# Performance work log

Measured on AMD Instinct MI355X. Metric: run time of the kernel, lower is better.

The kernel has to match this reference:

```python
import jax, jax.numpy as jnp
import numpy as np

NEG_SLOPE = 0.2  # LeakyReLU slope
PAD = 1          # padding for all 3x3 convs (kernel_size // 2)
K = 9            # 3x3 deformable kernel taps


def _conv2d(x, w, b):
    # x: (B,Cin,H,W), w: (Cout,Cin,3,3) -> (B,Cout,H,W), stride 1, SAME pad
    y = jax.lax.conv_general_dilated(x, w, (1, 1), 'SAME',
                                     dimension_numbers=('NCHW', 'OIHW', 'NCHW'))
    return y + b[None, :, None, None]


def _leaky(x):
    return jnp.where(x >= 0, x, NEG_SLOPE * x)


def _deform_conv(x, offset, w, b):
    # torchvision DeformConv2d, kernel 3x3, stride 1, pad 1, no modulation.
    # x: (B,C,H,W); offset: (B, 2*K, H, W) ordered (dy,dx) per tap; w: (O,C,3,3)
    B, C, H, W = x.shape
    O = w.shape[0]
    off = offset.reshape(B, K, 2, H, W)
    ks = jnp.arange(K)
    ky = (ks // 3).astype(x.dtype)
    kx = (ks % 3).astype(x.dtype)
    iy = jnp.arange(H, dtype=x.dtype)
    ix = jnp.arange(W, dtype=x.dtype)
    # sampling locations: out_pos + tap_pos - pad + learned offset  -> (B,K,H,W)
    py = iy[None, None, :, None] + ky[None, :, None, None] - PAD + off[:, :, 0]
    px = ix[None, None, None, :] + kx[None, :, None, None] - PAD + off[:, :, 1]

    y0 = jnp.floor(py)
    x0 = jnp.floor(px)
    wy = py - y0
    wx = px - x0
    y0i = y0.astype(jnp.int32)
    x0i = x0.astype(jnp.int32)

    def gather(img, yi, xi):  # img: (C,H,W); yi,xi: (K,H,W) -> (C,K,H,W)
        return img[:, yi, xi]
    vgather = jax.vmap(gather)  # over batch

    def corner(yi, xi, wgt):
        valid = (yi >= 0) & (yi < H) & (xi >= 0) & (xi < W)
        yc = jnp.clip(yi, 0, H - 1)
        xc = jnp.clip(xi, 0, W - 1)
        v = vgather(x, yc, xc)  # (B,C,K,H,W)
        return v * (wgt * valid.astype(x.dtype))[:, None]

    val = (corner(y0i, x0i, (1 - wy) * (1 - wx))
           + corner(y0i, x0i + 1, (1 - wy) * wx)
           + corner(y0i + 1, x0i, wy * (1 - wx))
           + corner(y0i + 1, x0i + 1, wy * wx))  # (B,C,K,H,W)
    out = jnp.einsum('bckhw,ock->bohw', val, w.reshape(O, C, K))
    return out + b[None, :, None, None]


def _stage(x, cw, cb, ow, ob, dw, db):
    h = _leaky(_conv2d(x, cw, cb))      # plain conv + LeakyReLU
    off = _conv2d(h, ow, ob)            # offset prediction (18 channels)
    return _leaky(_deform_conv(h, off, dw, db))


def setup_inputs() -> dict:
    key = jax.random.key(0)
    keys = iter(jax.random.split(key, 32))

    def nrm(shape, scale):
        return jax.random.normal(next(keys), shape, jnp.float32) * scale

    inp = {'x': jax.random.normal(next(keys), (4, 64, 128, 128), jnp.float32)}
    specs = [(64, 128), (128, 128), (128, 64)]
    for i, (ci, co) in enumerate(specs, 1):
        inp[f's{i}_cw'] = nrm((co, ci, 3, 3), (ci * 9) ** -0.5)
        inp[f's{i}_cb'] = jnp.zeros((co,), jnp.float32)
        inp[f's{i}_ow'] = nrm((18, co, 3, 3), 0.1 * (co * 9) ** -0.5)  # small offsets
        inp[f's{i}_ob'] = jnp.zeros((18,), jnp.float32)
        inp[f's{i}_dw'] = nrm((co, co, 3, 3), (co * 9) ** -0.5)
        inp[f's{i}_db'] = jnp.zeros((co,), jnp.float32)
    return inp


def reference(x,
              s1_cw, s1_cb, s1_ow, s1_ob, s1_dw, s1_db,
              s2_cw, s2_cb, s2_ow, s2_ob, s2_dw, s2_db,
              s3_cw, s3_cb, s3_ow, s3_ob, s3_dw, s3_db):
    x = _stage(x, s1_cw, s1_cb, s1_ow, s1_ob, s1_dw, s1_db)
    x = _stage(x, s2_cw, s2_cb, s2_ow, s2_ob, s2_dw, s2_db)
    x = _stage(x, s3_cw, s3_cb, s3_ow, s3_ob, s3_dw, s3_db)
    return x
```

## Files before the change

kernel.cpp:

```cpp
#include <hip/hip_runtime.h>
#include <hip/hip_bf16.h>

#define HW 128
#define HW2 16384
#define NEG 0.2f

typedef __attribute__((ext_vector_type(8))) short short8;
typedef __attribute__((ext_vector_type(4))) float f32x4;
typedef __attribute__((ext_vector_type(2))) float f32x2;

__device__ __forceinline__ float lrelu(float v) { return v >= 0.f ? v : NEG * v; }
__device__ __forceinline__ unsigned short f2bf(float f) {
    unsigned int u = __float_as_uint(f);
    u = (u + 0x7fffu + ((u >> 16) & 1u)) >> 16;
    return (unsigned short)u;
}
__device__ __forceinline__ unsigned int pk2(float a, float b) {
    __hip_bfloat162 h = __float22bfloat162_rn(float2{a, b});
    return *(unsigned int*)&h;
}
__device__ __forceinline__ float2 upk(unsigned int u) {
    return float2{__uint_as_float(u << 16), __uint_as_float(u & 0xffff0000u)};
}
__device__ __forceinline__ f32x2 upkv(unsigned int u) {
    f32x2 r;
    r.x = __uint_as_float(u << 16);
    r.y = __uint_as_float(u & 0xffff0000u);
    return r;
}

struct WSeg { const float* s; unsigned short* d; int K9; int NMT; int validM; int n; };
struct WArgs { WSeg seg[9]; };

__global__ void wrepack_kernel(WArgs a)
{
    const WSeg sg = a.seg[blockIdx.y];
    int i = blockIdx.x * 256 + threadIdx.x;
    if (i >= sg.n) return;
    int cl = i & 7, lane = (i >> 3) & 63;
    int rest = i >> 9;
    int mt = rest % sg.NMT, gs = rest / sg.NMT;
    int st = gs % 3, g = gs / 3;
    int quad = lane >> 4, l15 = lane & 15;
    int co = mt * 16 + l15, tap = st * 4 + quad;
    unsigned short v = 0;
    if (tap < 9 && co < sg.validM)
        v = f2bf(sg.s[(size_t)co * sg.K9 + (g * 8 + cl) * 9 + tap]);
    sg.d[i] = v;
}

template <int MTW, int SRCF>
__global__ __launch_bounds__(256, 4) void fused_conv(
    const void* __restrict__ actv, const unsigned short* __restrict__ wpad,
    const float* __restrict__ bias, unsigned short* __restrict__ outb,
    float* __restrict__ outf, int Cin, int Cout, int mode)
{
    constexpr int PB = 136 * 16;
    constexpr int SMB = 64 * 136 * 2;
    __shared__ char smem[SMB];
    unsigned short* Es = (unsigned short*)smem;

    const int t = threadIdx.x;
    const int tile = blockIdx.x, b = blockIdx.z;
    const int lane = t & 63, wv = t >> 6, quad = lane >> 4, l15 = lane & 15;
    const int y0 = (tile >> 2) * 2, x0 = (tile & 3) * 32;
    const int ngrp = Cin >> 3;
    const int NSTR = (Cout >> 4) * 512;

    const bool sok = lane < 34;
    const int gy = y0 - 1 + wv, gx = x0 - 1 + lane;
    const bool pok = sok && gy >= 0 && gy < HW && gx >= 0 && gx < HW;
    const int gp = pok ? gy * HW + gx : 0;
    const int slot = wv * 34 + lane;

    const float* actf = (const float*)actv;
    const unsigned short* acth = (const unsigned short*)actv;
    const size_t bofs = (size_t)b * Cin * HW2;

    int baddr[3][4];
#pragma unroll
    for (int st = 0; st < 3; ++st) {
        int tap = st * 4 + quad; tap = tap > 8 ? 8 : tap;
        int ky = (tap * 11) >> 5, kx = tap - 3 * ky;
#pragma unroll
        for (int nt = 0; nt < 4; ++nt) {
            int p = nt * 16 + l15, ly = p >> 5, lx = p & 31;
            baddr[st][nt] = ((ly + ky) * 34 + lx + kx) * 16;
        }
    }
    size_t abase[MTW];
#pragma unroll
    for (int m = 0; m < MTW; ++m)
        abase[m] = (size_t)((wv * MTW + m) * 512 + lane * 8);

    f32x4 acc[MTW][4];
#pragma unroll
    for (int m = 0; m < MTW; ++m)
#pragma unroll
        for (int nt = 0; nt < 4; ++nt) acc[m][nt] = (f32x4)(0.f);

    auto load_grp = [&](int g) -> uint4 {
        uint4 u; u.x = u.y = u.z = u.w = 0;
        if (!pok) return u;
        if (SRCF == 1) {
            u = *(const uint4*)(acth + bofs + ((size_t)g * HW2 + gp) * 8);
        } else {
            const float* pl = actf + bofs + (size_t)(g * 8) * HW2 + gp;
            float v0 = pl[0], v1 = pl[HW2], v2 = pl[2 * HW2], v3 = pl[3 * HW2];
            float v4 = pl[4 * HW2], v5 = pl[5 * HW2], v6 = pl[6 * HW2], v7 = pl[7 * HW2];
            u.x = pk2(v0, v1); u.y = pk2(v2, v3);
            u.z = pk2(v4, v5); u.w = pk2(v6, v7);
        }
        return u;
    };

    short8 apre[MTW][3];
    auto loadA = [&](int g) {
#pragma unroll
        for (int st = 0; st < 3; ++st)
#pragma unroll
            for (int m = 0; m < MTW; ++m)
                apre[m][st] = *(const short8*)(wpad + (size_t)(g * 3 + st) * NSTR + abase[m]);
    };

    uint4 cur = load_grp(0);
    if (sok) *(uint4*)(smem + slot * 16) = cur;
    loadA(0);
    if (ngrp > 1) cur = load_grp(1);
    __syncthreads();

    for (int g = 0; g < ngrp; ++g) {
        char* pb = smem + (g & 1) * PB;
#pragma unroll
        for (int st = 0; st < 3; ++st) {
            short8 bfr[4];
#pragma unroll
            for (int nt = 0; nt < 4; ++nt)
                bfr[nt] = *(const short8*)(pb + baddr[st][nt]);
#pragma unroll
            for (int m = 0; m < MTW; ++m) {
                short8 a = apre[m][st];
#pragma unroll
                for (int nt = 0; nt < 4; ++nt)
                    acc[m][nt] = __builtin_amdgcn_mfma_f32_16x16x32_bf16(
                        a, bfr[nt], acc[m][nt], 0, 0, 0);
            }
        }
        if (g + 1 < ngrp) {
            if (sok) *(uint4*)(smem + ((g + 1) & 1) * PB + slot * 16) = cur;
            loadA(g + 1);
            if (g + 2 < ngrp) cur = load_grp(g + 2);
        }
        __syncthreads();
    }

    if (mode == 0) {
        constexpr int ESTR = 136;
#pragma unroll
        for (int m = 0; m < MTW; ++m) {
            int cb = (wv * MTW + m) * 16;
#pragma unroll
            for (int nt = 0; nt < 4; ++nt) {
                int px = nt * 16 + l15;
                int co = cb + quad * 4;
                unsigned int u0 = pk2(lrelu(acc[m][nt][0] + bias[co]),
                                      lrelu(acc[m][nt][1] + bias[co + 1]));
                unsigned int u1 = pk2(lrelu(acc[m][nt][2] + bias[co + 2]),
                                      lrelu(acc[m][nt][3] + bias[co + 3]));
                uint2 u; u.x = u0; u.y = u1;
                *(uint2*)&Es[px * ESTR + co] = u;
            }
        }
        __syncthreads();
        const int ng8 = Cout >> 3;
        unsigned short* ob = outb + (size_t)b * Cout * HW2;
        for (int tt = t; tt < 64 * ng8; tt += 256) {
            int cg = tt >> 6, px = tt & 63;
            int gp2 = (y0 + (px >> 5)) * HW + x0 + (px & 31);
            *(uint4*)(ob + ((size_t)cg * HW2 + gp2) * 8) =
                *(const uint4*)&Es[px * ESTR + cg * 8];
        }
    } else {
        float* of = outf + (size_t)b * 18 * HW2;
#pragma unroll
        for (int m = 0; m < MTW; ++m) {
            int cb = (wv * MTW + m) * 16;
#pragma unroll
            for (int nt = 0; nt < 4; ++nt) {
                int px = nt * 16 + l15;
                int gp2 = (y0 + (px >> 5)) * HW + x0 + (px & 31);
#pragma unroll
                for (int r = 0; r < 4; ++r) {
                    int co = cb + quad * 4 + r;
                    if (co < 18)
                        of[(size_t)co * HW2 + gp2] = acc[m][nt][r] + bias[co];
                }
            }
        }
    }
}

template <int MTW>
__global__ __launch_bounds__(256, 4) void fused_deform(
    const unsigned short* __restrict__ acth,
    const unsigned short* __restrict__ woff, const float* __restrict__ obias,
    const unsigned short* __restrict__ wpad, const float* __restrict__ bias,
    unsigned short* __restrict__ outb, float* __restrict__ outf,
    int Cin, int Cout, int mode)
{
    constexpr int PATW = 43, PATR = 8, PATP = PATR * PATW;
    constexpr int CSTR = 104;
    constexpr int PB = PATP * 16;
    constexpr int CB = 64 * CSTR * 2;
    constexpr int SMB = 2 * PB + 2 * CB;
    constexpr int OPB = 136 * 16;
    __shared__ char smem[SMB];
    unsigned short* Es = (unsigned short*)smem;

    const int t = threadIdx.x;
    const int tile = blockIdx.x, b = blockIdx.z;
    const int lane = t & 63, wv = t >> 6, quad = lane >> 4, l15 = lane & 15;
    const int y0 = (tile >> 2) * 2, x0 = (tile & 3) * 32;
    const int ngrp = Cin >> 3;
    const int NSTR = (Cout >> 4) * 512;
    const int py0 = y0 - 3, px0 = x0 - 5;
    const size_t bofs = (size_t)b * Cin * HW2;

    for (int i = t; i < 384; i += 256) {
        int bu = i / 192;
        int ii = i - 192 * bu;
        int p = ii / 3, j = ii - 3 * p;
        uint4 z; z.x = z.y = z.z = z.w = 0;
        *(uint4*)(smem + 2 * PB + bu * CB + (p * CSTR + 72 + j * 8) * 2) = z;
    }

    {
        float* offbuf = (float*)(smem + 2 * OPB);
        const bool asok = lane < 34;
        const int agy = y0 - 1 + wv, agx = x0 - 1 + lane;
        const bool apok = asok && agy >= 0 && agy < HW && agx >= 0 && agx < HW;
        const int agp = apok ? agy * HW + agx : 0;
        const int aslot = wv * 34 + lane;

        const int mtile = wv & 1, npair = wv >> 1;
        int obad[3][2];
#pragma unroll
        for (int st = 0; st < 3; ++st) {
            int tap = st * 4 + quad; tap = tap > 8 ? 8 : tap;
            int ky = (tap * 11) >> 5, kx = tap - 3 * ky;
#pragma unroll
            for (int nn = 0; nn < 2; ++nn) {
                int p = (2 * npair + nn) * 16 + l15, ly = p >> 5, lx = p & 31;
                obad[st][nn] = ((ly + ky) * 34 + lx + kx) * 16;
            }
        }
        const size_t oa0 = (size_t)(mtile * 512 + lane * 8);

        f32x4 oacc[2];
        oacc[0] = (f32x4)(0.f); oacc[1] = (f32x4)(0.f);
        short8 oapre[3];
        auto loadAO = [&](int g) {
#pragma unroll
            for (int st = 0; st < 3; ++st)
                oapre[st] = *(const short8*)(woff + (size_t)(g * 3 + st) * 1024 + oa0);
        };
        auto load_g = [&](int g) -> uint4 {
            uint4 u; u.x = u.y = u.z = u.w = 0;
            if (apok) u = *(const uint4*)(acth + bofs + ((size_t)g * HW2 + agp) * 8);
            return u;
        };

        uint4 cur = load_g(0);
        if (asok) *(uint4*)(smem + aslot * 16) = cur;
        loadAO(0);
        if (ngrp > 1) cur = load_g(1);
        __syncthreads();

        for (int g = 0; g < ngrp; ++g) {
            const char* pb = smem + (g & 1) * OPB;
#pragma unroll
            for (int st = 0; st < 3; ++st) {
                short8 a = oapre[st];
#pragma unroll
                for (int nn = 0; nn < 2; ++nn) {
                    short8 bf = *(const short8*)(pb + obad[st][nn]);
                    oacc[nn] = __builtin_amdgcn_mfma_f32_16x16x32_bf16(
                        a, bf, oacc[nn], 0, 0, 0);
                }
            }
            if (g + 1 < ngrp) {
                if (asok) *(uint4*)(smem + ((g + 1) & 1) * OPB + aslot * 16) = cur;
                loadAO(g + 1);
                if (g + 2 < ngrp) cur = load_g(g + 2);
            }
            __syncthreads();
        }

        {
            int co0 = mtile * 16 + quad * 4;
            if (co0 < 18) {
#pragma unroll
                for (int nn = 0; nn < 2; ++nn) {
                    int px = (2 * npair + nn) * 16 + l15;
#pragma unroll
                    for (int r = 0; r < 4; ++r)
                        if (co0 + r < 18)
                            offbuf[px * 20 + co0 + r] = oacc[nn][r] + obias[co0 + r];
                }
            }
        }
        __syncthreads();
    }
    const float* offbuf = (const float*)(smem + 2 * OPB);

    float w00[3], w01[3], w10[3], w11[3];
    int pbase[3], csad[3], svalid[3];
    int allin = 1;
    {
#pragma unroll
        for (int s = 0; s < 3; ++s) {
            int task = t + s * 256;
            svalid[s] = task < 576;
            int task2 = svalid[s] ? task : 0;
            int p = task2 / 9, k = task2 - 9 * p;
            int yy = y0 + (p >> 5), xx = x0 + (p & 31);
            float2 dd = *(const float2*)(offbuf + p * 20 + 2 * k);
            float dy = dd.x, dx = dd.y;
            float py = (float)(yy + k / 3 - 1) + dy;
            float px = (float)(xx + k % 3 - 1) + dx;
            float fy = floorf(py), fx = floorf(px);
            float wy = py - fy, wx = px - fx;
            int iy = (int)fy, ix = (int)fx;
            w00[s] = (1.f - wy) * (1.f - wx);
            w01[s] = (1.f - wy) * wx;
            w10[s] = wy * (1.f - wx);
            w11[s] = wy * wx;
            pbase[s] = ((iy - py0) * PATW + (ix - px0)) * 16;
            csad[s] = (p * CSTR + k * 8) * 2;
            bool ip = iy >= py0 && iy + 1 <= py0 + (PATR - 1)
                   && ix >= px0 && ix + 1 <= px0 + (PATW - 1);
            if (!ip) allin = 0;
        }
    }
    const int fast = __syncthreads_and(allin);

    const int s0 = wv * 86 + lane;
    const int r0 = s0 / PATW, c0_ = s0 - PATW * r0;
    const int gy0_ = py0 + r0, gx0_ = px0 + c0_;
    const bool ok0 = gy0_ >= 0 && gy0_ < HW && gx0_ >= 0 && gx0_ < HW;
    const int go0 = ok0 ? gy0_ * HW + gx0_ : 0;
    const bool has1 = lane < 22;
    const int s1 = wv * 86 + 64 + lane;
    const int r1 = s1 / PATW, c1_ = s1 - PATW * r1;
    const int gy1_ = py0 + r1, gx1_ = px0 + c1_;
    const bool ok1 = has1 && gy1_ >= 0 && gy1_ < HW && gx1_ >= 0 && gx1_ < HW;
    const int go1 = ok1 ? gy1_ * HW + gx1_ : 0;

    size_t abase[MTW];
#pragma unroll
    for (int m = 0; m < MTW; ++m)
        abase[m] = (size_t)((wv * MTW + m) * 512 + lane * 8);
    const int bb0 = l15 * (CSTR * 2) + quad * 16;

    f32x4 acc[MTW][4];
#pragma unroll
    for (int m = 0; m < MTW; ++m)
#pragma unroll
        for (int nt = 0; nt < 4; ++nt) acc[m][nt] = (f32x4)(0.f);

    short8 apre[MTW][3];
    auto loadA = [&](int g) {
#pragma unroll
        for (int st = 0; st < 3; ++st)
#pragma unroll
            for (int m = 0; m < MTW; ++m)
                apre[m][st] = *(const short8*)(wpad + (size_t)(g * 3 + st) * NSTR + abase[m]);
    };

    auto mfma_pre = [&](const char* cs) {
#pragma unroll
        for (int st = 0; st < 3; ++st) {
            short8 bfr[4];
#pragma unroll
            for (int nt = 0; nt < 4; ++nt)
                bfr[nt] = *(const short8*)(cs + bb0 + nt * 16 * (CSTR * 2) + st * 64);
#pragma unroll
            for (int m = 0; m < MTW; ++m) {
                short8 a = apre[m][st];
#pragma unroll
                for (int nt = 0; nt < 4; ++nt)
                    acc[m][nt] = __builtin_amdgcn_mfma_f32_16x16x32_bf16(
                        a, bfr[nt], acc[m][nt], 0, 0, 0);
            }
        }
    };

    if (fast) {
        uint4 u0, u1;
        u0.x = u0.y = u0.z = u0.w = 0; u1 = u0;
        if (ok0) u0 = *(const uint4*)(acth + bofs + (size_t)go0 * 8);
        if (ok1) u1 = *(const uint4*)(acth + bofs + (size_t)go1 * 8);
        *(uint4*)(smem + s0 * 16) = u0;
        if (has1) *(uint4*)(smem + s1 * 16) = u1;
        if (ngrp > 1) {
            u0.x = u0.y = u0.z = u0.w = 0; u1 = u0;
            if (ok0) u0 = *(const uint4*)(acth + bofs + ((size_t)HW2 + go0) * 8);
            if (ok1) u1 = *(const uint4*)(acth + bofs + ((size_t)HW2 + go1) * 8);
        }
        __syncthreads();

        for (int g = 0; g < ngrp; ++g) {
            const char* pb = smem + (g & 1) * PB;
            char* csW = smem + 2 * PB + (g & 1) * CB;

            if (g > 0)
                mfma_pre(smem + 2 * PB + ((g - 1) & 1) * CB);

#pragma unroll
            for (int s = 0; s < 3; ++s) {
                if (!svalid[s]) continue;
                const char* base = pb + pbase[s];
                uint4 c00 = *(const uint4*)base;
                uint4 c01 = *(const uint4*)(base + 16);
                uint4 c10 = *(const uint4*)(base + PATW * 16);
                uint4 c11 = *(const uint4*)(base + PATW * 16 + 16);
                f32x2 vw0 = (f32x2)(w00[s]), vw1 = (f32x2)(w01[s]);
                f32x2 vw2 = (f32x2)(w10[s]), vw3 = (f32x2)(w11[s]);
                f32x2 a0 = vw0 * upkv(c00.x) + vw1 * upkv(c01.x)
                         + vw2 * upkv(c10.x) + vw3 * upkv(c11.x);
                f32x2 a1 = vw0 * upkv(c00.y) + vw1 * upkv(c01.y)
                         + vw2 * upkv(c10.y) + vw3 * upkv(c11.y);
                f32x2 a2 = vw0 * upkv(c00.z) + vw1 * upkv(c01.z)
                         + vw2 * upkv(c10.z) + vw3 * upkv(c11.z);
                f32x2 a3 = vw0 * upkv(c00.w) + vw1 * upkv(c01.w)
                         + vw2 * upkv(c10.w) + vw3 * upkv(c11.w);
                uint4 ou;
                ou.x = pk2(a0.x, a0.y); ou.y = pk2(a1.x, a1.y);
                ou.z = pk2(a2.x, a2.y); ou.w = pk2(a3.x, a3.y);
                *(uint4*)(csW + csad[s]) = ou;
            }

            if (g + 1 < ngrp) {
                char* pn = smem + ((g + 1) & 1) * PB;
                *(uint4*)(pn + s0 * 16) = u0;
                if (has1) *(uint4*)(pn + s1 * 16) = u1;
            }
            loadA(g);
            if (g + 2 < ngrp) {
                u0.x = u0.y = u0.z = u0.w = 0; u1 = u0;
                if (ok0) u0 = *(const uint4*)(acth + bofs +
                                              ((size_t)(g + 2) * HW2 + go0) * 8);
                if (ok1) u1 = *(const uint4*)(acth + bofs +
                                              ((size_t)(g + 2) * HW2 + go1) * 8);
            }
            __syncthreads();
        }
        mfma_pre(smem + 2 * PB + ((ngrp - 1) & 1) * CB);
    } else {
        char* csW = smem + 2 * PB;
        for (int g = 0; g < ngrp; ++g) {
            const unsigned short* gb = acth + bofs + (size_t)g * HW2 * 8;
#pragma unroll
            for (int s = 0; s < 3; ++s) {
                if (!svalid[s]) continue;
                int task = t + s * 256;
                int p = task / 9, k = task - 9 * p;
                int yy = y0 + (p >> 5), xx = x0 + (p & 31);
                float2 dd = *(const float2*)(offbuf + p * 20 + 2 * k);
                float dy = dd.x, dx = dd.y;
                float py = (float)(yy + k / 3 - 1) + dy;
                float px = (float)(xx + k % 3 - 1) + dx;
                float fy = floorf(py), fx = floorf(px);
                float wy = py - fy, wx = px - fx;
                int iy = (int)fy, ix = (int)fx;
                float f0 = 0, f1 = 0, f2 = 0, f3 = 0, f4 = 0, f5 = 0, f6 = 0, f7 = 0;
#pragma unroll
                for (int q = 0; q < 4; ++q) {
                    int ddy = q >> 1, ddx = q & 1;
                    int sy = iy + ddy, sx = ix + ddx;
                    float w = (ddy ? wy : 1.f - wy) * (ddx ? wx : 1.f - wx);
                    if (sy < 0 || sy >= HW || sx < 0 || sx >= HW) w = 0.f;
                    int cy = min(max(sy, 0), HW - 1), cx = min(max(sx, 0), HW - 1);
                    uint4 c = *(const uint4*)(gb + (size_t)(cy * HW + cx) * 8);
                    float2 p0 = upk(c.x), p1 = upk(c.y), p2 = upk(c.z), p3 = upk(c.w);
                    f0 += w * p0.x; f1 += w * p0.y; f2 += w * p1.x; f3 += w * p1.y;
                    f4 += w * p2.x; f5 += w * p2.y; f6 += w * p3.x; f7 += w * p3.y;
                }
                uint4 ou;
                ou.x = pk2(f0, f1); ou.y = pk2(f2, f3);
                ou.z = pk2(f4, f5); ou.w = pk2(f6, f7);
                *(uint4*)(csW + csad[s]) = ou;
            }
            __syncthreads();
            loadA(g);
            mfma_pre(csW);
            __syncthreads();
        }
    }

    __syncthreads();
    if (mode == 0) {
        constexpr int ESTR = 136;
#pragma unroll
        for (int m = 0; m < MTW; ++m) {
            int cb = (wv * MTW + m) * 16;
#pragma unroll
            for (int nt = 0; nt < 4; ++nt) {
                int px = nt * 16 + l15;
                int co = cb + quad * 4;
                unsigned int u0 = pk2(lrelu(acc[m][nt][0] + bias[co]),
                                      lrelu(acc[m][nt][1] + bias[co + 1]));
                unsigned int u1 = pk2(lrelu(acc[m][nt][2] + bias[co + 2]),
                                      lrelu(acc[m][nt][3] + bias[co + 3]));
                uint2 u; u.x = u0; u.y = u1;
                *(uint2*)&Es[px * ESTR + co] = u;
            }
        }
        __syncthreads();
        const int ng8 = Cout >> 3;
        unsigned short* ob = outb + (size_t)b * Cout * HW2;
        for (int tt = t; tt < 64 * ng8; tt += 256) {
            int cg = tt >> 6, px = tt & 63;
            int gp2 = (y0 + (px >> 5)) * HW + x0 + (px & 31);
            *(uint4*)(ob + ((size_t)cg * HW2 + gp2) * 8) =
                *(const uint4*)&Es[px * ESTR + cg * 8];
        }
    } else {
        float* of = outf + (size_t)b * Cout * HW2;
#pragma unroll
        for (int m = 0; m < MTW; ++m) {
            int cb = (wv * MTW + m) * 16;
#pragma unroll
            for (int nt = 0; nt < 4; ++nt) {
                int px = nt * 16 + l15;
                int gp2 = (y0 + (px >> 5)) * HW + x0 + (px & 31);
#pragma unroll
                for (int r = 0; r < 4; ++r) {
                    int co = cb + quad * 4 + r;
                    of[(size_t)co * HW2 + gp2] = lrelu(acc[m][nt][r] + bias[co]);
                }
            }
        }
    }
}

extern "C" void kernel_launch(void* const* d_in, const int* in_sizes, int n_in,
                              void* d_out, int out_size, void* d_ws,
                              size_t ws_size, hipStream_t stream)
{
    const float* x = (const float*)d_in[0];
    const float* p[18];
    for (int i = 0; i < 18; ++i) p[i] = (const float*)d_in[1 + i];

    char* ws = (char*)d_ws;
    unsigned short* A1 = (unsigned short*)ws;
    unsigned short* A2 = (unsigned short*)(ws + 16777216);
    unsigned short* WB = (unsigned short*)(ws + 38273024);

    unsigned short* Wc1 = WB;
    unsigned short* Wo1 = Wc1 + 98304;
    unsigned short* Wd1 = Wo1 + 98304;
    unsigned short* Wc2 = Wd1 + 196608;
    unsigned short* Wo2 = Wc2 + 196608;
    unsigned short* Wd2 = Wo2 + 98304;
    unsigned short* Wc3 = Wd2 + 196608;
    unsigned short* Wo3 = Wc3 + 98304;
    unsigned short* Wd3 = Wo3 + 49152;

    WArgs wa;
    wa.seg[0] = {p[0],  Wc1,  576, 8, 128,  98304};
    wa.seg[1] = {p[2],  Wo1, 1152, 2,  18,  49152};
    wa.seg[2] = {p[4],  Wd1, 1152, 8, 128, 196608};
    wa.seg[3] = {p[6],  Wc2, 1152, 8, 128, 196608};
    wa.seg[4] = {p[8],  Wo2, 1152, 2,  18,  49152};
    wa.seg[5] = {p[10], Wd2, 1152, 8, 128, 196608};
    wa.seg[6] = {p[12], Wc3, 1152, 4,  64,  98304};
    wa.seg[7] = {p[14], Wo3,  576, 2,  18,  24576};
    wa.seg[8] = {p[16], Wd3,  576, 4,  64,  49152};
    wrepack_kernel<<<dim3(768, 9), 256, 0, stream>>>(wa);

    dim3 g(256, 1, 4);
    fused_conv<2, 0><<<g, 256, 0, stream>>>(x, Wc1, p[1], A1, nullptr, 64, 128, 0);
    fused_deform<2><<<g, 256, 0, stream>>>(A1, Wo1, p[3], Wd1, p[5], A2, nullptr, 128, 128, 0);
    fused_conv<2, 1><<<g, 256, 0, stream>>>(A2, Wc2, p[7], A1, nullptr, 128, 128, 0);
    fused_deform<2><<<g, 256, 0, stream>>>(A1, Wo2, p[9], Wd2, p[11], A2, nullptr, 128, 128, 0);
    fused_conv<1, 1><<<g, 256, 0, stream>>>(A2, Wc3, p[13], A1, nullptr, 128, 64, 0);
    fused_deform<1><<<g, 256, 0, stream>>>(A1, Wo3, p[15], Wd3, p[17], nullptr, (float*)d_out, 64, 64, 1);
}
```

Before: 300.3 us.

## Load offset-conv input directly from global instead of LDS double buffer

```diff
diff --git a/kernel.cpp b/kernel.cpp
--- a/kernel.cpp
+++ b/kernel.cpp
@@ -236,77 +236,50 @@
 
     {
         float* offbuf = (float*)(smem + 2 * OPB);
-        const bool asok = lane < 34;
-        const int agy = y0 - 1 + wv, agx = x0 - 1 + lane;
-        const bool apok = asok && agy >= 0 && agy < HW && agx >= 0 && agx < HW;
-        const int agp = apok ? agy * HW + agx : 0;
-        const int aslot = wv * 34 + lane;
-
         const int mtile = wv & 1, npair = wv >> 1;
-        int obad[3][2];
+        int bok[3][2], bga[3][2];
 #pragma unroll
         for (int st = 0; st < 3; ++st) {
             int tap = st * 4 + quad; tap = tap > 8 ? 8 : tap;
             int ky = (tap * 11) >> 5, kx = tap - 3 * ky;
 #pragma unroll
             for (int nn = 0; nn < 2; ++nn) {
-                int p = (2 * npair + nn) * 16 + l15, ly = p >> 5, lx = p & 31;
-                obad[st][nn] = ((ly + ky) * 34 + lx + kx) * 16;
+                int p = (2 * npair + nn) * 16 + l15;
+                int sy = y0 + (p >> 5) + ky - 1, sx = x0 + (p & 31) + kx - 1;
+                bok[st][nn] = sy >= 0 && sy < HW && sx >= 0 && sx < HW;
+                bga[st][nn] = bok[st][nn] ? (sy * HW + sx) * 8 : 0;
             }
         }
         const size_t oa0 = (size_t)(mtile * 512 + lane * 8);
-
         f32x4 oacc[2];
         oacc[0] = (f32x4)(0.f); oacc[1] = (f32x4)(0.f);
-        short8 oapre[3];
-        auto loadAO = [&](int g) {
+        for (int g = 0; g < ngrp; ++g) {
+            const unsigned short* gb = acth + bofs + (size_t)g * (HW2 * 8);
+            short8 a[3], bf[3][2];
+#pragma unroll
+            for (int st = 0; st < 3; ++st) {
+                a[st] = *(const short8*)(woff + (size_t)(g * 3 + st) * 1024 + oa0);
+#pragma unroll
+                for (int nn = 0; nn < 2; ++nn)
+                    bf[st][nn] = bok[st][nn]
+                        ? *(const short8*)(gb + bga[st][nn]) : (short8)(short)0;
+            }
 #pragma unroll
             for (int st = 0; st < 3; ++st)
-                oapre[st] = *(const short8*)(woff + (size_t)(g * 3 + st) * 1024 + oa0);
-        };
-        auto load_g = [&](int g) -> uint4 {
-            uint4 u; u.x = u.y = u.z = u.w = 0;
-            if (apok) u = *(const uint4*)(acth + bofs + ((size_t)g * HW2 + agp) * 8);
-            return u;
-        };
-
-        uint4 cur = load_g(0);
-        if (asok) *(uint4*)(smem + aslot * 16) = cur;
-        loadAO(0);
-        if (ngrp > 1) cur = load_g(1);
-        __syncthreads();
-
-        for (int g = 0; g < ngrp; ++g) {
-            const char* pb = smem + (g & 1) * OPB;
-#pragma unroll
-            for (int st = 0; st < 3; ++st) {
-                short8 a = oapre[st];
-#pragma unroll
-                for (int nn = 0; nn < 2; ++nn) {
-                    short8 bf = *(const short8*)(pb + obad[st][nn]);
+#pragma unroll
+                for (int nn = 0; nn < 2; ++nn)
                     oacc[nn] = __builtin_amdgcn_mfma_f32_16x16x32_bf16(
-                        a, bf, oacc[nn], 0, 0, 0);
-                }
-            }
-            if (g + 1 < ngrp) {
-                if (asok) *(uint4*)(smem + ((g + 1) & 1) * OPB + aslot * 16) = cur;
-                loadAO(g + 1);
-                if (g + 2 < ngrp) cur = load_g(g + 2);
-            }
-            __syncthreads();
-        }
-
-        {
-            int co0 = mtile * 16 + quad * 4;
-            if (co0 < 18) {
-#pragma unroll
-                for (int nn = 0; nn < 2; ++nn) {
-                    int px = (2 * npair + nn) * 16 + l15;
-#pragma unroll
-                    for (int r = 0; r < 4; ++r)
-                        if (co0 + r < 18)
-                            offbuf[px * 20 + co0 + r] = oacc[nn][r] + obias[co0 + r];
-                }
+                        a[st], bf[st][nn], oacc[nn], 0, 0, 0);
+        }
+        int co0 = mtile * 16 + quad * 4;
+        if (co0 < 18) {
+#pragma unroll
+            for (int nn = 0; nn < 2; ++nn) {
+                int px = (2 * npair + nn) * 16 + l15;
+#pragma unroll
+                for (int r = 0; r < 4; ++r)
+                    if (co0 + r < 18)
+                        offbuf[px * 20 + co0 + r] = oacc[nn][r] + obias[co0 + r];
             }
         }
         __syncthreads();
```

Result: slower. 327.1 us (+8.9%).

## Stage all input channel groups in LDS upfront, dropping per-group barriers

Applied to the files above, without the earlier changes.

```diff
diff --git a/kernel.cpp b/kernel.cpp
--- a/kernel.cpp
+++ b/kernel.cpp
@@ -56,7 +56,7 @@
     float* __restrict__ outf, int Cin, int Cout, int mode)
 {
     constexpr int PB = 136 * 16;
-    constexpr int SMB = 64 * 136 * 2;
+    constexpr int SMB = 16 * PB;
     __shared__ char smem[SMB];
     unsigned short* Es = (unsigned short*)smem;
 
@@ -123,14 +123,21 @@
                 apre[m][st] = *(const short8*)(wpad + (size_t)(g * 3 + st) * NSTR + abase[m]);
     };
 
-    uint4 cur = load_grp(0);
-    if (sok) *(uint4*)(smem + slot * 16) = cur;
+    for (int gc = 0; gc < ngrp; gc += 4) {
+        uint4 u0 = load_grp(gc),     u1 = load_grp(gc + 1);
+        uint4 u2 = load_grp(gc + 2), u3 = load_grp(gc + 3);
+        if (sok) {
+            *(uint4*)(smem + (gc + 0) * PB + slot * 16) = u0;
+            *(uint4*)(smem + (gc + 1) * PB + slot * 16) = u1;
+            *(uint4*)(smem + (gc + 2) * PB + slot * 16) = u2;
+            *(uint4*)(smem + (gc + 3) * PB + slot * 16) = u3;
+        }
+    }
     loadA(0);
-    if (ngrp > 1) cur = load_grp(1);
     __syncthreads();
 
     for (int g = 0; g < ngrp; ++g) {
-        char* pb = smem + (g & 1) * PB;
+        const char* pb = smem + g * PB;
 #pragma unroll
         for (int st = 0; st < 3; ++st) {
             short8 bfr[4];
@@ -146,13 +153,9 @@
                         a, bfr[nt], acc[m][nt], 0, 0, 0);
             }
         }
-        if (g + 1 < ngrp) {
-            if (sok) *(uint4*)(smem + ((g + 1) & 1) * PB + slot * 16) = cur;
-            loadA(g + 1);
-            if (g + 2 < ngrp) cur = load_grp(g + 2);
-        }
-        __syncthreads();
-    }
+        if (g + 1 < ngrp) loadA(g + 1);
+    }
+    __syncthreads();
 
     if (mode == 0) {
         constexpr int ESTR = 136;
@@ -226,22 +229,30 @@
     const int py0 = y0 - 3, px0 = x0 - 5;
     const size_t bofs = (size_t)b * Cin * HW2;
 
-    for (int i = t; i < 384; i += 256) {
-        int bu = i / 192;
-        int ii = i - 192 * bu;
-        int p = ii / 3, j = ii - 3 * p;
-        uint4 z; z.x = z.y = z.z = z.w = 0;
-        *(uint4*)(smem + 2 * PB + bu * CB + (p * CSTR + 72 + j * 8) * 2) = z;
-    }
-
     {
-        float* offbuf = (float*)(smem + 2 * OPB);
         const bool asok = lane < 34;
         const int agy = y0 - 1 + wv, agx = x0 - 1 + lane;
         const bool apok = asok && agy >= 0 && agy < HW && agx >= 0 && agx < HW;
         const int agp = apok ? agy * HW + agx : 0;
         const int aslot = wv * 34 + lane;
 
+        for (int gc = 0; gc < ngrp; gc += 4) {
+            uint4 u0, u1, u2, u3;
+            u0.x = u0.y = u0.z = u0.w = 0; u1 = u0; u2 = u0; u3 = u0;
+            if (apok) {
+                u0 = *(const uint4*)(acth + bofs + ((size_t)(gc + 0) * HW2 + agp) * 8);
+                u1 = *(const uint4*)(acth + bofs + ((size_t)(gc + 1) * HW2 + agp) * 8);
+                u2 = *(const uint4*)(acth + bofs + ((size_t)(gc + 2) * HW2 + agp) * 8);
+                u3 = *(const uint4*)(acth + bofs + ((size_t)(gc + 3) * HW2 + agp) * 8);
+            }
+            if (asok) {
+                *(uint4*)(smem + (gc + 0) * OPB + aslot * 16) = u0;
+                *(uint4*)(smem + (gc + 1) * OPB + aslot * 16) = u1;
+                *(uint4*)(smem + (gc + 2) * OPB + aslot * 16) = u2;
+                *(uint4*)(smem + (gc + 3) * OPB + aslot * 16) = u3;
+            }
+        }
+
         const int mtile = wv & 1, npair = wv >> 1;
         int obad[3][2];
 #pragma unroll
@@ -259,25 +270,13 @@
         f32x4 oacc[2];
         oacc[0] = (f32x4)(0.f); oacc[1] = (f32x4)(0.f);
         short8 oapre[3];
-        auto loadAO = [&](int g) {
-#pragma unroll
-            for (int st = 0; st < 3; ++st)
-                oapre[st] = *(const short8*)(woff + (size_t)(g * 3 + st) * 1024 + oa0);
-        };
-        auto load_g = [&](int g) -> uint4 {
-            uint4 u; u.x = u.y = u.z = u.w = 0;
-            if (apok) u = *(const uint4*)(acth + bofs + ((size_t)g * HW2 + agp) * 8);
-            return u;
-        };
-
-        uint4 cur = load_g(0);
-        if (asok) *(uint4*)(smem + aslot * 16) = cur;
-        loadAO(0);
-        if (ngrp > 1) cur = load_g(1);
+#pragma unroll
+        for (int st = 0; st < 3; ++st)
+            oapre[st] = *(const short8*)(woff + (size_t)st * 1024 + oa0);
         __syncthreads();
 
         for (int g = 0; g < ngrp; ++g) {
-            const char* pb = smem + (g & 1) * OPB;
+            const char* pb = smem + g * OPB;
 #pragma unroll
             for (int st = 0; st < 3; ++st) {
                 short8 a = oapre[st];
@@ -289,24 +288,24 @@
                 }
             }
             if (g + 1 < ngrp) {
-                if (asok) *(uint4*)(smem + ((g + 1) & 1) * OPB + aslot * 16) = cur;
-                loadAO(g + 1);
-                if (g + 2 < ngrp) cur = load_g(g + 2);
-            }
-            __syncthreads();
-        }
-
-        {
-            int co0 = mtile * 16 + quad * 4;
-            if (co0 < 18) {
-#pragma unroll
-                for (int nn = 0; nn < 2; ++nn) {
-                    int px = (2 * npair + nn) * 16 + l15;
-#pragma unroll
-                    for (int r = 0; r < 4; ++r)
-                        if (co0 + r < 18)
-                            offbuf[px * 20 + co0 + r] = oacc[nn][r] + obias[co0 + r];
-                }
+#pragma unroll
+                for (int st = 0; st < 3; ++st)
+                    oapre[st] = *(const short8*)(
+                        woff + (size_t)((g + 1) * 3 + st) * 1024 + oa0);
+            }
+        }
+        __syncthreads();
+
+        float* offbuf = (float*)(smem + 2 * OPB);
+        int co0 = mtile * 16 + quad * 4;
+        if (co0 < 18) {
+#pragma unroll
+            for (int nn = 0; nn < 2; ++nn) {
+                int px = (2 * npair + nn) * 16 + l15;
+#pragma unroll
+                for (int r = 0; r < 4; ++r)
+                    if (co0 + r < 18)
+                        offbuf[px * 20 + co0 + r] = oacc[nn][r] + obias[co0 + r];
             }
         }
         __syncthreads();
@@ -344,6 +343,14 @@
     }
     const int fast = __syncthreads_and(allin);
 
+    for (int i = t; i < 384; i += 256) {
+        int bu = i / 192;
+        int ii = i - 192 * bu;
+        int p = ii / 3, j = ii - 3 * p;
+        uint4 z; z.x = z.y = z.z = z.w = 0;
+        *(uint4*)(smem + 2 * PB + bu * CB + (p * CSTR + 72 + j * 8) * 2) = z;
+    }
+
     const int s0 = wv * 86 + lane;
     const int r0 = s0 / PATW, c0_ = s0 - PATW * r0;
     const int gy0_ = py0 + r0, gx0_ = px0 + c0_;
```

Result: no change. 305.3 us (+1.7%).

## Gather deform corners directly from global memory instead of staging LDS patch

Applied to the files above, without the earlier changes.

```diff
diff --git a/kernel.cpp b/kernel.cpp
--- a/kernel.cpp
+++ b/kernel.cpp
@@ -208,12 +208,11 @@
     unsigned short* __restrict__ outb, float* __restrict__ outf,
     int Cin, int Cout, int mode)
 {
-    constexpr int PATW = 43, PATR = 8, PATP = PATR * PATW;
     constexpr int CSTR = 104;
-    constexpr int PB = PATP * 16;
     constexpr int CB = 64 * CSTR * 2;
-    constexpr int SMB = 2 * PB + 2 * CB;
     constexpr int OPB = 136 * 16;
+    constexpr int CSB = 2 * OPB + 5120;
+    constexpr int SMB = CSB + 2 * CB;
     __shared__ char smem[SMB];
     unsigned short* Es = (unsigned short*)smem;
 
@@ -223,7 +222,6 @@
     const int y0 = (tile >> 2) * 2, x0 = (tile & 3) * 32;
     const int ngrp = Cin >> 3;
     const int NSTR = (Cout >> 4) * 512;
-    const int py0 = y0 - 3, px0 = x0 - 5;
     const size_t bofs = (size_t)b * Cin * HW2;
 
     for (int i = t; i < 384; i += 256) {
@@ -231,7 +229,7 @@
         int ii = i - 192 * bu;
         int p = ii / 3, j = ii - 3 * p;
         uint4 z; z.x = z.y = z.z = z.w = 0;
-        *(uint4*)(smem + 2 * PB + bu * CB + (p * CSTR + 72 + j * 8) * 2) = z;
+        *(uint4*)(smem + CSB + bu * CB + (p * CSTR + 72 + j * 8) * 2) = z;
     }
 
     {
@@ -314,8 +312,7 @@
     const float* offbuf = (const float*)(smem + 2 * OPB);
 
     float w00[3], w01[3], w10[3], w11[3];
-    int pbase[3], csad[3], svalid[3];
-    int allin = 1;
+    int cof0[3], cof1[3], cof2[3], cof3[3], csad[3], svalid[3];
     {
 #pragma unroll
         for (int s = 0; s < 3; ++s) {
@@ -331,30 +328,23 @@
             float fy = floorf(py), fx = floorf(px);
             float wy = py - fy, wx = px - fx;
             int iy = (int)fy, ix = (int)fx;
-            w00[s] = (1.f - wy) * (1.f - wx);
-            w01[s] = (1.f - wy) * wx;
-            w10[s] = wy * (1.f - wx);
-            w11[s] = wy * wx;
-            pbase[s] = ((iy - py0) * PATW + (ix - px0)) * 16;
+            float W0 = (1.f - wy) * (1.f - wx);
+            float W1 = (1.f - wy) * wx;
+            float W2 = wy * (1.f - wx);
+            float W3 = wy * wx;
+            auto corner = [&](int sy, int sx, float& w) -> int {
+                if (sy < 0 || sy >= HW || sx < 0 || sx >= HW) w = 0.f;
+                int cy = min(max(sy, 0), HW - 1), cx = min(max(sx, 0), HW - 1);
+                return (cy * HW + cx) * 16;
+            };
+            cof0[s] = corner(iy, ix, W0);
+            cof1[s] = corner(iy, ix + 1, W1);
+            cof2[s] = corner(iy + 1, ix, W2);
+            cof3[s] = corner(iy + 1, ix + 1, W3);
+            w00[s] = W0; w01[s] = W1; w10[s] = W2; w11[s] = W3;
             csad[s] = (p * CSTR + k * 8) * 2;
-            bool ip = iy >= py0 && iy + 1 <= py0 + (PATR - 1)
-                   && ix >= px0 && ix + 1 <= px0 + (PATW - 1);
-            if (!ip) allin = 0;
-        }
-    }
-    const int fast = __syncthreads_and(allin);
-
-    const int s0 = wv * 86 + lane;
-    const int r0 = s0 / PATW, c0_ = s0 - PATW * r0;
-    const int gy0_ = py0 + r0, gx0_ = px0 + c0_;
-    const bool ok0 = gy0_ >= 0 && gy0_ < HW && gx0_ >= 0 && gx0_ < HW;
-    const int go0 = ok0 ? gy0_ * HW + gx0_ : 0;
-    const bool has1 = lane < 22;
-    const int s1 = wv * 86 + 64 + lane;
-    const int r1 = s1 / PATW, c1_ = s1 - PATW * r1;
-    const int gy1_ = py0 + r1, gx1_ = px0 + c1_;
-    const bool ok1 = has1 && gy1_ >= 0 && gy1_ < HW && gx1_ >= 0 && gx1_ < HW;
-    const int go1 = ok1 ? gy1_ * HW + gx1_ : 0;
+        }
+    }
 
     size_t abase[MTW];
 #pragma unroll
@@ -395,108 +385,47 @@
         }
     };
 
-    if (fast) {
-        uint4 u0, u1;
-        u0.x = u0.y = u0.z = u0.w = 0; u1 = u0;
-        if (ok0) u0 = *(const uint4*)(acth + bofs + (size_t)go0 * 8);
-        if (ok1) u1 = *(const uint4*)(acth + bofs + (size_t)go1 * 8);
-        *(uint4*)(smem + s0 * 16) = u0;
-        if (has1) *(uint4*)(smem + s1 * 16) = u1;
-        if (ngrp > 1) {
-            u0.x = u0.y = u0.z = u0.w = 0; u1 = u0;
-            if (ok0) u0 = *(const uint4*)(acth + bofs + ((size_t)HW2 + go0) * 8);
-            if (ok1) u1 = *(const uint4*)(acth + bofs + ((size_t)HW2 + go1) * 8);
-        }
+    for (int g = 0; g < ngrp; ++g) {
+        const char* gb = (const char*)(acth + bofs + (size_t)g * (HW2 * 8));
+        uint4 cc[3][4];
+#pragma unroll
+        for (int s = 0; s < 3; ++s)
+            if (svalid[s]) {
+                cc[s][0] = *(const uint4*)(gb + cof0[s]);
+                cc[s][1] = *(const uint4*)(gb + cof1[s]);
+                cc[s][2] = *(const uint4*)(gb + cof2[s]);
+                cc[s][3] = *(const uint4*)(gb + cof3[s]);
+            }
+
+        if (g > 0)
+            mfma_pre(smem + CSB + ((g - 1) & 1) * CB);
+
+        char* csW = smem + CSB + (g & 1) * CB;
+#pragma unroll
+        for (int s = 0; s < 3; ++s) {
+            if (!svalid[s]) continue;
+            uint4 c00 = cc[s][0], c01 = cc[s][1];
+            uint4 c10 = cc[s][2], c11 = cc[s][3];
+            f32x2 vw0 = (f32x2)(w00[s]), vw1 = (f32x2)(w01[s]);
+            f32x2 vw2 = (f32x2)(w10[s]), vw3 = (f32x2)(w11[s]);
+            f32x2 a0 = vw0 * upkv(c00.x) + vw1 * upkv(c01.x)
+                     + vw2 * upkv(c10.x) + vw3 * upkv(c11.x);
+            f32x2 a1 = vw0 * upkv(c00.y) + vw1 * upkv(c01.y)
+                     + vw2 * upkv(c10.y) + vw3 * upkv(c11.y);
+            f32x2 a2 = vw0 * upkv(c00.z) + vw1 * upkv(c01.z)
+                     + vw2 * upkv(c10.z) + vw3 * upkv(c11.z);
+            f32x2 a3 = vw0 * upkv(c00.w) + vw1 * upkv(c01.w)
+                     + vw2 * upkv(c10.w) + vw3 * upkv(c11.w);
+            uint4 ou;
+            ou.x = pk2(a0.x, a0.y); ou.y = pk2(a1.x, a1.y);
+            ou.z = pk2(a2.x, a2.y); ou.w = pk2(a3.x, a3.y);
+            *(uint4*)(csW + csad[s]) = ou;
+        }
+
+        loadA(g);
         __syncthreads();
-
-        for (int g = 0; g < ngrp; ++g) {
-            const char* pb = smem + (g & 1) * PB;
-            char* csW = smem + 2 * PB + (g & 1) * CB;
-
-            if (g > 0)
-                mfma_pre(smem + 2 * PB + ((g - 1) & 1) * CB);
-
-#pragma unroll
-            for (int s = 0; s < 3; ++s) {
-                if (!svalid[s]) continue;
-                const char* base = pb + pbase[s];
-                uint4 c00 = *(const uint4*)base;
-                uint4 c01 = *(const uint4*)(base + 16);
-                uint4 c10 = *(const uint4*)(base + PATW * 16);
-                uint4 c11 = *(const uint4*)(base + PATW * 16 + 16);
-                f32x2 vw0 = (f32x2)(w00[s]), vw1 = (f32x2)(w01[s]);
-                f32x2 vw2 = (f32x2)(w10[s]), vw3 = (f32x2)(w11[s]);
-                f32x2 a0 = vw0 * upkv(c00.x) + vw1 * upkv(c01.x)
-                         + vw2 * upkv(c10.x) + vw3 * upkv(c11.x);
-                f32x2 a1 = vw0 * upkv(c00.y) + vw1 * upkv(c01.y)
-                         + vw2 * upkv(c10.y) + vw3 * upkv(c11.y);
-                f32x2 a2 = vw0 * upkv(c00.z) + vw1 * upkv(c01.z)
-                         + vw2 * upkv(c10.z) + vw3 * upkv(c11.z);
-                f32x2 a3 = vw0 * upkv(c00.w) + vw1 * upkv(c01.w)
-                         + vw2 * upkv(c10.w) + vw3 * upkv(c11.w);
-                uint4 ou;
-                ou.x = pk2(a0.x, a0.y); ou.y = pk2(a1.x, a1.y);
-                ou.z = pk2(a2.x, a2.y); ou.w = pk2(a3.x, a3.y);
-                *(uint4*)(csW + csad[s]) = ou;
-            }
-
-            if (g + 1 < ngrp) {
-                char* pn = smem + ((g + 1) & 1) * PB;
-                *(uint4*)(pn + s0 * 16) = u0;
-                if (has1) *(uint4*)(pn + s1 * 16) = u1;
-            }
-            loadA(g);
-            if (g + 2 < ngrp) {
-                u0.x = u0.y = u0.z = u0.w = 0; u1 = u0;
-                if (ok0) u0 = *(const uint4*)(acth + bofs +
-                                              ((size_t)(g + 2) * HW2 + go0) * 8);
-                if (ok1) u1 = *(const uint4*)(acth + bofs +
-                                              ((size_t)(g + 2) * HW2 + go1) * 8);
-            }
-            __syncthreads();
-        }
-        mfma_pre(smem + 2 * PB + ((ngrp - 1) & 1) * CB);
-    } else {
-        char* csW = smem + 2 * PB;
-        for (int g = 0; g < ngrp; ++g) {
-            const unsigned short* gb = acth + bofs + (size_t)g * HW2 * 8;
-#pragma unroll
-            for (int s = 0; s < 3; ++s) {
-                if (!svalid[s]) continue;
-                int task = t + s * 256;
-                int p = task / 9, k = task - 9 * p;
-                int yy = y0 + (p >> 5), xx = x0 + (p & 31);
-                float2 dd = *(const float2*)(offbuf + p * 20 + 2 * k);
-                float dy = dd.x, dx = dd.y;
-                float py = (float)(yy + k / 3 - 1) + dy;
-                float px = (float)(xx + k % 3 - 1) + dx;
-                float fy = floorf(py), fx = floorf(px);
-                float wy = py - fy, wx = px - fx;
-                int iy = (int)fy, ix = (int)fx;
-                float f0 = 0, f1 = 0, f2 = 0, f3 = 0, f4 = 0, f5 = 0, f6 = 0, f7 = 0;
-#pragma unroll
-                for (int q = 0; q < 4; ++q) {
-                    int ddy = q >> 1, ddx = q & 1;
-                    int sy = iy + ddy, sx = ix + ddx;
-                    float w = (ddy ? wy : 1.f - wy) * (ddx ? wx : 1.f - wx);
-                    if (sy < 0 || sy >= HW || sx < 0 || sx >= HW) w = 0.f;
-                    int cy = min(max(sy, 0), HW - 1), cx = min(max(sx, 0), HW - 1);
-                    uint4 c = *(const uint4*)(gb + (size_t)(cy * HW + cx) * 8);
-                    float2 p0 = upk(c.x), p1 = upk(c.y), p2 = upk(c.z), p3 = upk(c.w);
-                    f0 += w * p0.x; f1 += w * p0.y; f2 += w * p1.x; f3 += w * p1.y;
-                    f4 += w * p2.x; f5 += w * p2.y; f6 += w * p3.x; f7 += w * p3.y;
-                }
-                uint4 ou;
-                ou.x = pk2(f0, f1); ou.y = pk2(f2, f3);
-                ou.z = pk2(f4, f5); ou.w = pk2(f6, f7);
-                *(uint4*)(csW + csad[s]) = ou;
-            }
-            __syncthreads();
-            loadA(g);
-            mfma_pre(csW);
-            __syncthreads();
-        }
-    }
+    }
+    mfma_pre(smem + CSB + ((ngrp - 1) & 1) * CB);
 
     __syncthreads();
     if (mode == 0) {
```

Measured after the change: 457.1 us. 1.52x slower.
